# Performance work log

Measured on AMD Instinct MI355X. Metric: run time of the kernel, lower is better.

The kernel has to match this reference:

```python
import jax, jax.numpy as jnp
import numpy as np

N = 100000
E = 3200000
IN_C, NHID, OUT_C, K = 256, 128, 40, 2


def gcn_norm(src, dst, ew, n):
    # add self loops with weight 1.0 (PyG gcn_norm default, add_self_loops=True)
    loop = jnp.arange(n, dtype=src.dtype)
    src = jnp.concatenate([src, loop])
    dst = jnp.concatenate([dst, loop])
    ew = jnp.concatenate([ew, jnp.ones((n,), dtype=ew.dtype)])
    deg = jax.ops.segment_sum(ew, dst, num_segments=n)
    dinv = jnp.where(deg > 0, jax.lax.rsqrt(deg), 0.0)
    norm = dinv[src] * ew * dinv[dst]
    return src, dst, norm


def sgconv(x, src, dst, norm, W, b, k, n):
    # x' = (D^-1/2 (A+I) D^-1/2)^k x, then linear
    for _ in range(k):
        x = jax.ops.segment_sum(x[src] * norm[:, None], dst, num_segments=n)
    return x @ W + b


def setup_inputs() -> dict:
    key = jax.random.key(0)
    ks = jax.random.split(key, 8)
    x = jax.random.normal(ks[0], (N, IN_C), dtype=jnp.float32)
    edge_index = jax.random.randint(ks[1], (2, E), 0, N, dtype=jnp.int64)
    edge_weight = jax.random.uniform(ks[2], (E,), dtype=jnp.float32)
    s1 = 1.0 / np.sqrt(IN_C)
    s2 = 1.0 / np.sqrt(NHID)
    W1 = jax.random.uniform(ks[3], (IN_C, NHID), minval=-s1, maxval=s1, dtype=jnp.float32)
    b1 = jax.random.uniform(ks[4], (NHID,), minval=-s1, maxval=s1, dtype=jnp.float32)
    W2 = jax.random.uniform(ks[5], (NHID, OUT_C), minval=-s2, maxval=s2, dtype=jnp.float32)
    b2 = jax.random.uniform(ks[6], (OUT_C,), minval=-s2, maxval=s2, dtype=jnp.float32)
    return {"x": x, "edge_index": edge_index, "edge_weight": edge_weight,
            "W1": W1, "b1": b1, "W2": W2, "b2": b2}


def reference(x, edge_index, edge_weight, W1, b1, W2, b2):
    n = x.shape[0]
    src, dst, norm = gcn_norm(edge_index[0], edge_index[1], edge_weight, n)
    h = jax.nn.relu(sgconv(x, src, dst, norm, W1, b1, K, n))
    # dropout is identity in eval mode (training=False)
    out = sgconv(h, src, dst, norm, W2, b2, K, n)
    return jax.nn.log_softmax(out, axis=1)
```

## Files before the change

kernel.cpp:

```cpp
#include <hip/hip_runtime.h>
#include <math.h>


constexpr int IN_C = 256, NHID = 128, OUT_C = 40;
constexpr int BSHIFT = 8;
constexpr int BNODES = 256;
constexpr int BCAP = 16128;
constexpr int MAXB = 400;
typedef unsigned int u32;
typedef unsigned short u16;
typedef unsigned char u8;
typedef __attribute__((ext_vector_type(8))) short bf16x8;
typedef __attribute__((ext_vector_type(4))) float f32x4;

__device__ inline u16 f2bf(float f) {
    u32 u = __float_as_uint(f);
    return (u16)((u + 0x7FFF + ((u >> 16) & 1)) >> 16);
}
__device__ inline int nlo4(u32 v) { return ((int)(v << 28)) >> 28; }
__device__ inline int nhi4(u32 v) { return ((int)(v << 24)) >> 28; }

__global__ __launch_bounds__(256) void k_bucketize(const int* __restrict__ src,
                                                   const int* __restrict__ dst,
                                                   const float* __restrict__ ew,
                                                   int* __restrict__ bcur,
                                                   int2* __restrict__ bbuf,
                                                   int E, int nbins) {
    __shared__ int hist[MAXB];
    __shared__ int base[MAXB];
    int tid = threadIdx.x;
    int chunk = (E + gridDim.x - 1) / gridDim.x;
    int e0 = blockIdx.x * chunk;
    int e1 = min(E, e0 + chunk);
    for (int i = tid; i < nbins; i += 256) hist[i] = 0;
    __syncthreads();
    for (int e = e0 + tid; e < e1; e += 256)
        atomicAdd(&hist[dst[e] >> BSHIFT], 1);
    __syncthreads();
    for (int i = tid; i < nbins; i += 256) {
        int c = hist[i];
        base[i] = c ? atomicAdd(&bcur[i], c) : 0;
        hist[i] = 0;
    }
    __syncthreads();
    for (int e = e0 + tid; e < e1; e += 256) {
        int d = dst[e];
        int b = d >> BSHIFT;
        int r = atomicAdd(&hist[b], 1);
        int pos = base[b] + r;
        if (pos < BCAP) {
            int meta = src[e] | ((d & (BNODES - 1)) << 17);
            bbuf[(size_t)b * BCAP + pos] = make_int2(meta, __float_as_int(ew[e]));
        }
    }
}

__global__ __launch_bounds__(256) void k_bcnt_deg(const int2* __restrict__ bbuf,
                                                  const int* __restrict__ bcur,
                                                  int* __restrict__ cnt,
                                                  float* __restrict__ dinv,
                                                  float* __restrict__ selfnorm, int N) {
    __shared__ int hist[BNODES];
    __shared__ int dsum[BNODES];
    int b = blockIdx.x;
    int tid = threadIdx.x;
    hist[tid] = 0; dsum[tid] = 0;
    __syncthreads();
    int c = min(bcur[b], BCAP);
    const int2* p = bbuf + (size_t)b * BCAP;
    for (int e = tid; e < c; e += 256) {
        int2 rec = p[e];
        int dl = rec.x >> 17;
        atomicAdd(&hist[dl], 1);
        atomicAdd(&dsum[dl], (int)rintf(__int_as_float(rec.y) * 8388608.0f));
    }
    __syncthreads();
    int node = b * BNODES + tid;
    if (node < N) {
        cnt[node] = hist[tid];
        float d = (float)dsum[tid] * (1.0f / 8388608.0f) + 1.0f;
        dinv[node] = rsqrtf(d);
        selfnorm[node] = 1.0f / d;
    }
}

__global__ __launch_bounds__(256) void k_scan_part(const int* __restrict__ cnt,
                                                   int* __restrict__ partial, int N) {
    __shared__ int sh[256];
    int i = blockIdx.x * 256 + threadIdx.x;
    sh[threadIdx.x] = (i < N) ? cnt[i] : 0;
    __syncthreads();
    for (int off = 128; off > 0; off >>= 1) {
        if (threadIdx.x < off) sh[threadIdx.x] += sh[threadIdx.x + off];
        __syncthreads();
    }
    if (threadIdx.x == 0) partial[blockIdx.x] = sh[0];
}

__global__ __launch_bounds__(512) void k_scan_top(int* __restrict__ partial, int nb) {
    __shared__ int sh[512];
    int t = threadIdx.x;
    int v = (t < nb) ? partial[t] : 0;
    sh[t] = v;
    __syncthreads();
    for (int off = 1; off < 512; off <<= 1) {
        int add = (t >= off) ? sh[t - off] : 0;
        __syncthreads();
        sh[t] += add;
        __syncthreads();
    }
    if (t < nb) partial[t] = sh[t] - v;
}

__global__ __launch_bounds__(256) void k_scan_apply(const int* __restrict__ cnt,
                                                    const int* __restrict__ partial,
                                                    int* __restrict__ row_start, int N) {
    __shared__ int sh[256];
    int i = blockIdx.x * 256 + threadIdx.x;
    int v = (i < N) ? cnt[i] : 0;
    sh[threadIdx.x] = v;
    __syncthreads();
    for (int off = 1; off < 256; off <<= 1) {
        int add = (threadIdx.x >= off) ? sh[threadIdx.x - off] : 0;
        __syncthreads();
        sh[threadIdx.x] += add;
        __syncthreads();
    }
    if (i < N) row_start[i] = sh[threadIdx.x] - v + partial[blockIdx.x];
}

__global__ __launch_bounds__(256) void k_place(const int2* __restrict__ bbuf,
                                               const int* __restrict__ bcur,
                                               const int* __restrict__ row_start,
                                               const float* __restrict__ dinv,
                                               int2* __restrict__ csr, int N) {
    __shared__ int rs[BNODES];
    __shared__ int cur[BNODES];
    __shared__ float dv[BNODES];
    int b = blockIdx.x;
    int tid = threadIdx.x;
    int node = b * BNODES + tid;
    rs[tid] = (node < N) ? row_start[node] : 0;
    dv[tid] = (node < N) ? dinv[node] : 0.f;
    cur[tid] = 0;
    __syncthreads();
    int c = min(bcur[b], BCAP);
    const int2* p = bbuf + (size_t)b * BCAP;
    for (int e = tid; e < c; e += 256) {
        int2 rec = p[e];
        int dl = rec.x >> 17;
        int s = rec.x & 0x1FFFF;
        float w = dinv[s] * __int_as_float(rec.y) * dv[dl];
        int r = atomicAdd(&cur[dl], 1);
        csr[rs[dl] + r] = make_int2(s, __float_as_int(w));
    }
}

__global__ __launch_bounds__(256) void k_wconv(const float* __restrict__ W,
                                               u16* __restrict__ Wc) {
    int o = blockIdx.x * 256 + threadIdx.x;
    if (o < IN_C * NHID) {
        int j = o & 7, col = (o >> 3) & 127, c = o >> 10;
        Wc[o] = f2bf(W[(size_t)(c * 8 + j) * NHID + col]);
    }
}

__global__ __launch_bounds__(256) void k_gmax(const float* __restrict__ v, int n,
                                              int* __restrict__ gm) {
    __shared__ float sm[4];
    float m = 0.f;
    for (int i = blockIdx.x * 256 + threadIdx.x; i < n; i += 256 * 256)
        m = fmaxf(m, v[i]);
#pragma unroll
    for (int o = 32; o > 0; o >>= 1) m = fmaxf(m, __shfl_xor(m, o, 64));
    if ((threadIdx.x & 63) == 0) sm[threadIdx.x >> 6] = m;
    __syncthreads();
    if (threadIdx.x == 0) {
        m = fmaxf(fmaxf(sm[0], sm[1]), fmaxf(sm[2], sm[3]));
        atomicMax(gm, __float_as_int(m));
    }
}

__global__ __launch_bounds__(256) void k_gemm1(const float* __restrict__ X,
                                               const u16* __restrict__ Wc,
                                               u16* __restrict__ Yq,
                                               float* __restrict__ Ys, int N) {
    int tid = threadIdx.x;
    int wv = tid >> 6, lane = tid & 63;
    int q = lane >> 4, r16 = lane & 15;
    int row = blockIdx.x * 64 + wv * 16 + r16;
    int rowc = min(row, N - 1);
    const float* xp = X + (size_t)rowc * IN_C + q * 8;
    f32x4 acc[8];
#pragma unroll
    for (int i = 0; i < 8; ++i) acc[i] = (f32x4){0.f, 0.f, 0.f, 0.f};
#pragma unroll
    for (int ks = 0; ks < 8; ++ks) {
        float4 a0 = *(const float4*)(xp + ks * 32);
        float4 a1 = *(const float4*)(xp + ks * 32 + 4);
        bf16x8 xf;
        xf[0] = (short)f2bf(a0.x); xf[1] = (short)f2bf(a0.y);
        xf[2] = (short)f2bf(a0.z); xf[3] = (short)f2bf(a0.w);
        xf[4] = (short)f2bf(a1.x); xf[5] = (short)f2bf(a1.y);
        xf[6] = (short)f2bf(a1.z); xf[7] = (short)f2bf(a1.w);
        int c = ks * 4 + q;
#pragma unroll
        for (int ct = 0; ct < 8; ++ct) {
            bf16x8 wf = *(const bf16x8*)&Wc[(size_t)((c << 7) + ct * 16 + r16) << 3];
            acc[ct] = __builtin_amdgcn_mfma_f32_16x16x32_bf16(wf, xf, acc[ct], 0, 0, 0);
        }
    }
    float m = 0.f;
#pragma unroll
    for (int ct = 0; ct < 8; ++ct) {
        m = fmaxf(m, fmaxf(fmaxf(fabsf(acc[ct].x), fabsf(acc[ct].y)),
                           fmaxf(fabsf(acc[ct].z), fabsf(acc[ct].w))));
    }
    m = fmaxf(m, __shfl_xor(m, 16, 64));
    m = fmaxf(m, __shfl_xor(m, 32, 64));
    float qs = m > 0.f ? 7.0f / m : 0.f;
    if (row < N) {
        u16* yp = Yq + (size_t)row * 32;
#pragma unroll
        for (int ct = 0; ct < 8; ++ct) {
            int q0 = (int)rintf(acc[ct].x * qs);
            int q1 = (int)rintf(acc[ct].y * qs);
            int q2 = (int)rintf(acc[ct].z * qs);
            int q3 = (int)rintf(acc[ct].w * qs);
            u32 b0 = (q0 & 0xF) | ((q1 & 0xF) << 4);
            u32 b1_ = (q2 & 0xF) | ((q3 & 0xF) << 4);
            yp[ct * 4 + q] = (u16)(b0 | (b1_ << 8));
        }
        if (lane < 16) Ys[row] = m * (1.0f / 7.0f);
    }
}

__global__ __launch_bounds__(256) void k_gemm2(const u32* __restrict__ Hq,
                                               const float* __restrict__ Hs,
                                               const float* __restrict__ W2,
                                               const float* __restrict__ b1,
                                               u8* __restrict__ Tq,
                                               float* __restrict__ Ts, int N) {
    __shared__ float Ws[NHID * OUT_C];
    __shared__ float As[64][132];
    __shared__ float b1s[128];
    int tid = threadIdx.x;
    for (int idx = tid; idx < NHID * OUT_C; idx += 256) Ws[idx] = W2[idx];
    if (tid < 128) b1s[tid] = b1[tid];
    __syncthreads();
    int bm = blockIdx.x * 64;
#pragma unroll
    for (int j = 0; j < 4; ++j) {
        int idx = tid + j * 256;
        int r = idx >> 4, w = idx & 15;
        int grow = bm + r;
        float vals[8] = {};
        if (grow < N) {
            u32 v = Hq[(size_t)grow * 16 + w];
            float s = Hs[grow];
#pragma unroll
            for (int k = 0; k < 4; ++k) {
                u32 byte = (v >> (8 * k)) & 0xFF;
                vals[2 * k]     = s * (float)nlo4(byte);
                vals[2 * k + 1] = s * (float)nhi4(byte);
            }
        }
#pragma unroll
        for (int k = 0; k < 8; ++k)
            As[r][w * 8 + k] = fmaxf(vals[k] + b1s[w * 8 + k], 0.f);
    }
    __syncthreads();
    int r = tid >> 2;
    int c0 = (tid & 3) * 10;
    float acc[10] = {};
#pragma unroll 4
    for (int k = 0; k < NHID; ++k) {
        float a = As[r][k];
#pragma unroll
        for (int j = 0; j < 10; ++j) acc[j] += a * Ws[k * OUT_C + c0 + j];
    }
    float m = 0.f;
#pragma unroll
    for (int j = 0; j < 10; ++j) m = fmaxf(m, fabsf(acc[j]));
    m = fmaxf(m, __shfl_xor(m, 1, 64));
    m = fmaxf(m, __shfl_xor(m, 2, 64));
    float qs = m > 0.f ? 7.0f / m : 0.f;
    int grow = bm + r;
    if (grow < N) {
        u8* tp = Tq + (size_t)grow * 32 + (tid & 3) * 5;
#pragma unroll
        for (int j = 0; j < 5; ++j) {
            int q0 = (int)rintf(acc[2 * j] * qs);
            int q1 = (int)rintf(acc[2 * j + 1] * qs);
            tp[j] = (u8)((q0 & 0xF) | ((q1 & 0xF) << 4));
        }
        if ((tid & 3) == 0) Ts[grow] = m * (1.0f / 7.0f);
    }
}

__global__ __launch_bounds__(256) void k_prop128(const u8* __restrict__ in,
                                                 const float* __restrict__ ins,
                                                 u8* __restrict__ outq,
                                                 float* __restrict__ outs,
                                                 const int2* __restrict__ csr,
                                                 const int* __restrict__ row_start,
                                                 const int* __restrict__ cnt,
                                                 const float* __restrict__ selfnorm,
                                                 const int* __restrict__ gmaxi, int N) {
    __shared__ int2 stage[256];
    int tid = threadIdx.x;
    int wid = (blockIdx.x * 256 + tid) >> 6;
    int lane = tid & 63;
    int wb = tid & ~63;
    if (wid >= N) return;
    float gm = __int_as_float(*gmaxi);
    float S = gm > 0.f ? 524288.0f / gm : 0.f;
    float invS = gm * (1.0f / 524288.0f);
    int beg = row_start[wid], num = cnt[wid];
    int wqs = (int)rintf(selfnorm[wid] * ins[wid] * S);
    u32 xv = in[(size_t)wid * 64 + lane];
    int ax = wqs * nlo4(xv), ay = wqs * nhi4(xv);
    int bx = 0, by = 0;
    int e = beg, end = beg + num;
    while (e < end) {
        int m = min(64, end - e);
        int2 rec = csr[e + min(lane, m - 1)];
        int wq = (int)rintf(__int_as_float(rec.y) * ins[rec.x] * S);
        stage[wb + lane] = make_int2(rec.x, wq);
        int j = 0;
        for (; j + 8 <= m; j += 8) {
            int2 r0 = stage[wb + j + 0];
            int2 r1 = stage[wb + j + 1];
            int2 r2 = stage[wb + j + 2];
            int2 r3 = stage[wb + j + 3];
            int2 r4 = stage[wb + j + 4];
            int2 r5 = stage[wb + j + 5];
            int2 r6 = stage[wb + j + 6];
            int2 r7 = stage[wb + j + 7];
            u32 x0 = in[(size_t)r0.x * 64 + lane];
            u32 x1 = in[(size_t)r1.x * 64 + lane];
            u32 x2 = in[(size_t)r2.x * 64 + lane];
            u32 x3 = in[(size_t)r3.x * 64 + lane];
            u32 x4 = in[(size_t)r4.x * 64 + lane];
            u32 x5 = in[(size_t)r5.x * 64 + lane];
            u32 x6 = in[(size_t)r6.x * 64 + lane];
            u32 x7 = in[(size_t)r7.x * 64 + lane];
            ax += r0.y * nlo4(x0); ay += r0.y * nhi4(x0);
            bx += r1.y * nlo4(x1); by += r1.y * nhi4(x1);
            ax += r2.y * nlo4(x2); ay += r2.y * nhi4(x2);
            bx += r3.y * nlo4(x3); by += r3.y * nhi4(x3);
            ax += r4.y * nlo4(x4); ay += r4.y * nhi4(x4);
            bx += r5.y * nlo4(x5); by += r5.y * nhi4(x5);
            ax += r6.y * nlo4(x6); ay += r6.y * nhi4(x6);
            bx += r7.y * nlo4(x7); by += r7.y * nhi4(x7);
        }
        for (; j < m; ++j) {
            int2 r = stage[wb + j];
            u32 x = in[(size_t)r.x * 64 + lane];
            ax += r.y * nlo4(x); ay += r.y * nhi4(x);
        }
        e += m;
    }
    ax += bx; ay += by;
    float axf = (float)ax * invS, ayf = (float)ay * invS;
    float m2 = fmaxf(fabsf(axf), fabsf(ayf));
#pragma unroll
    for (int o = 32; o > 0; o >>= 1) m2 = fmaxf(m2, __shfl_xor(m2, o, 64));
    float qs = m2 > 0.f ? 7.0f / m2 : 0.f;
    int qx = (int)rintf(axf * qs), qy = (int)rintf(ayf * qs);
    outq[(size_t)wid * 64 + lane] = (u8)((qx & 0xF) | ((qy & 0xF) << 4));
    if (lane == 0) outs[wid] = m2 * (1.0f / 7.0f);
}

__device__ inline void prop40_body(const u8* __restrict__ in,
                                   const float* __restrict__ ins,
                                   const int2* __restrict__ csr,
                                   const int* __restrict__ row_start,
                                   const int* __restrict__ cnt,
                                   const float* __restrict__ selfnorm,
                                   int2* stage, int wb,
                                   int wid, int lane, float S,
                                   int& axo, int& ayo) {
    int half = lane >> 5, fl = lane & 31;
    bool act = fl < 20;
    int beg = row_start[wid], end = beg + cnt[wid];
    int ax = 0, ay = 0, bx = 0, by = 0;
    if (act && half == 0) {
        u32 u = in[(size_t)wid * 32 + fl];
        int wqs = (int)rintf(selfnorm[wid] * ins[wid] * S);
        ax = wqs * nlo4(u); ay = wqs * nhi4(u);
    }
    int e = beg;
    while (e < end) {
        int m = min(64, end - e);
        int2 rec = csr[e + min(lane, m - 1)];
        int wq = (int)rintf(__int_as_float(rec.y) * ins[rec.x] * S);
        stage[wb + lane] = make_int2(rec.x, wq);
        int j = 0;
        for (; j + 8 <= m; j += 8) {
            int2 r0 = stage[wb + j + half];
            int2 r1 = stage[wb + j + 2 + half];
            int2 r2 = stage[wb + j + 4 + half];
            int2 r3 = stage[wb + j + 6 + half];
            if (act) {
                u32 u0 = in[(size_t)r0.x * 32 + fl];
                u32 u1 = in[(size_t)r1.x * 32 + fl];
                u32 u2 = in[(size_t)r2.x * 32 + fl];
                u32 u3 = in[(size_t)r3.x * 32 + fl];
                ax += r0.y * nlo4(u0); ay += r0.y * nhi4(u0);
                bx += r1.y * nlo4(u1); by += r1.y * nhi4(u1);
                ax += r2.y * nlo4(u2); ay += r2.y * nhi4(u2);
                bx += r3.y * nlo4(u3); by += r3.y * nhi4(u3);
            }
        }
        for (; j + half < m; j += 2) {
            int2 r = stage[wb + j + half];
            if (act) {
                u32 u = in[(size_t)r.x * 32 + fl];
                ax += r.y * nlo4(u); ay += r.y * nhi4(u);
            }
        }
        e += m;
    }
    ax += bx; ay += by;
    ax += __shfl_xor(ax, 32, 64);
    ay += __shfl_xor(ay, 32, 64);
    axo = ax; ayo = ay;
}

__global__ __launch_bounds__(256) void k_prop40(const u8* __restrict__ in,
                                                const float* __restrict__ ins,
                                                u8* __restrict__ outq,
                                                float* __restrict__ outs,
                                                const int2* __restrict__ csr,
                                                const int* __restrict__ row_start,
                                                const int* __restrict__ cnt,
                                                const float* __restrict__ selfnorm,
                                                const int* __restrict__ gmaxi, int N) {
    __shared__ int2 stage[256];
    int tid = threadIdx.x;
    int wid = (blockIdx.x * 256 + tid) >> 6;
    int lane = tid & 63;
    if (wid >= N) return;
    float gm = __int_as_float(*gmaxi);
    float S = gm > 0.f ? 524288.0f / gm : 0.f;
    float invS = gm * (1.0f / 524288.0f);
    int ax, ay;
    prop40_body(in, ins, csr, row_start, cnt, selfnorm, stage, tid & ~63, wid, lane, S, ax, ay);
    int half = lane >> 5, fl = lane & 31;
    float axf = (float)ax * invS, ayf = (float)ay * invS;
    float m2 = fmaxf(fabsf(axf), fabsf(ayf));
    if (fl >= 20) m2 = 0.f;
#pragma unroll
    for (int o = 16; o > 0; o >>= 1) m2 = fmaxf(m2, __shfl_xor(m2, o, 64));
    float qs = m2 > 0.f ? 7.0f / m2 : 0.f;
    if (half == 0 && fl < 20) {
        int qx = (int)rintf(axf * qs), qy = (int)rintf(ayf * qs);
        outq[(size_t)wid * 32 + fl] = (u8)((qx & 0xF) | ((qy & 0xF) << 4));
        if (fl == 0) outs[wid] = m2 * (1.0f / 7.0f);
    }
}

__global__ __launch_bounds__(256) void k_prop40_lsm(const u8* __restrict__ in,
                                                    const float* __restrict__ ins,
                                                    float* __restrict__ out,
                                                    const int2* __restrict__ csr,
                                                    const int* __restrict__ row_start,
                                                    const int* __restrict__ cnt,
                                                    const float* __restrict__ selfnorm,
                                                    const float* __restrict__ b2,
                                                    const int* __restrict__ gmaxi, int N) {
    __shared__ int2 stage[256];
    int tid = threadIdx.x;
    int wid = (blockIdx.x * 256 + tid) >> 6;
    int lane = tid & 63;
    if (wid >= N) return;
    float gm = __int_as_float(*gmaxi);
    float S = gm > 0.f ? 524288.0f / gm : 0.f;
    float invS = gm * (1.0f / 524288.0f);
    int ax, ay;
    prop40_body(in, ins, csr, row_start, cnt, selfnorm, stage, tid & ~63, wid, lane, S, ax, ay);
    int half = lane >> 5, fl = lane & 31;
    bool act = fl < 20;
    float vx = -INFINITY, vy = -INFINITY;
    if (half == 0 && act) {
        vx = (float)ax * invS + b2[2 * fl];
        vy = (float)ay * invS + b2[2 * fl + 1];
    }
    float m2 = fmaxf(vx, vy);
#pragma unroll
    for (int o = 32; o > 0; o >>= 1) m2 = fmaxf(m2, __shfl_xor(m2, o, 64));
    float ex = (half == 0 && act) ? (__expf(vx - m2) + __expf(vy - m2)) : 0.f;
    float s = ex;
#pragma unroll
    for (int o = 32; o > 0; o >>= 1) s += __shfl_xor(s, o, 64);
    if (half == 0 && act) {
        float ls = logf(s);
        float2 o2 = make_float2(vx - m2 - ls, vy - m2 - ls);
        *(float2*)&out[(size_t)wid * 40 + 2 * fl] = o2;
    }
}

extern "C" void kernel_launch(void* const* d_in, const int* in_sizes, int n_in,
                              void* d_out, int out_size, void* d_ws, size_t ws_size,
                              hipStream_t stream) {
    const int N = in_sizes[0] / IN_C;
    const int E = in_sizes[2];
    const float* x  = (const float*)d_in[0];
    const int*   src = (const int*)d_in[1];
    const int*   dst = src + E;
    const float* ew = (const float*)d_in[2];
    const float* W1 = (const float*)d_in[3];
    const float* b1 = (const float*)d_in[4];
    const float* W2 = (const float*)d_in[5];
    const float* b2 = (const float*)d_in[6];
    float* out = (float*)d_out;

    char* p = (char*)d_ws;
    auto alloc = [&](size_t bytes) -> char* {
        char* r = p;
        p += (bytes + 255) & ~(size_t)255;
        return r;
    };
    float* dinv     = (float*)alloc((size_t)N * 4);
    float* selfnorm = (float*)alloc((size_t)N * 4);
    int*   cnt      = (int*)alloc((size_t)N * 4);
    int*   row_start= (int*)alloc((size_t)N * 4);
    int*   partial  = (int*)alloc(((N + 255) / 256) * 4);
    int*   bcur     = (int*)alloc(MAXB * 4);
    int*   gmax     = (int*)alloc(8 * 4);
    u16*   Wc       = (u16*)alloc((size_t)IN_C * NHID * 2);
    int2*  csr      = (int2*)alloc((size_t)E * 8);
    const int nbins = (N + BNODES - 1) >> BSHIFT;
    char*  region   = alloc((size_t)nbins * BCAP * 8);
    int2*  bbuf = (int2*)region;
    u8*    h4A  = (u8*)(region);
    u8*    h4B  = (u8*)(region + 7000000);
    u8*    t4A  = (u8*)(region + 14000000);
    u8*    t4B  = (u8*)(region + 17400000);
    float* sA   = (float*)(region + 20800000);
    float* sB   = (float*)(region + 21300000);
    float* tsA  = (float*)(region + 21800000);
    float* tsB  = (float*)(region + 22300000);

    hipMemsetAsync(bcur, 0, nbins * 4, stream);
    hipMemsetAsync(gmax, 0, 8 * 4, stream);

    int gn = (N + 255) / 256;
    int nb = gn;
    int gp = (N + 3) / 4;

    k_bucketize<<<256, 256, 0, stream>>>(src, dst, ew, bcur, bbuf, E, nbins);
    k_bcnt_deg<<<nbins, 256, 0, stream>>>(bbuf, bcur, cnt, dinv, selfnorm, N);
    k_scan_part<<<nb, 256, 0, stream>>>(cnt, partial, N);
    k_scan_top<<<1, 512, 0, stream>>>(partial, nb);
    k_scan_apply<<<nb, 256, 0, stream>>>(cnt, partial, row_start, N);
    k_place<<<nbins, 256, 0, stream>>>(bbuf, bcur, row_start, dinv, csr, N);
    k_wconv<<<(IN_C * NHID + 255) / 256, 256, 0, stream>>>(W1, Wc);

    k_gemm1<<<(N + 63) / 64, 256, 0, stream>>>(x, Wc, (u16*)h4A, sA, N);
    k_gmax<<<256, 256, 0, stream>>>(sA, N, &gmax[0]);

    k_prop128<<<gp, 256, 0, stream>>>(h4A, sA, h4B, sB, csr, row_start, cnt, selfnorm,
                                      &gmax[0], N);
    k_gmax<<<256, 256, 0, stream>>>(sB, N, &gmax[1]);
    k_prop128<<<gp, 256, 0, stream>>>(h4B, sB, h4A, sA, csr, row_start, cnt, selfnorm,
                                      &gmax[1], N);

    k_gemm2<<<(N + 63) / 64, 256, 0, stream>>>((const u32*)h4A, sA, W2, b1, t4A, tsA, N);
    k_gmax<<<256, 256, 0, stream>>>(tsA, N, &gmax[2]);

    k_prop40<<<gp, 256, 0, stream>>>(t4A, tsA, t4B, tsB, csr, row_start, cnt, selfnorm,
                                     &gmax[2], N);
    k_gmax<<<256, 256, 0, stream>>>(tsB, N, &gmax[3]);
    k_prop40_lsm<<<gp, 256, 0, stream>>>(t4B, tsB, out, csr, row_start, cnt, selfnorm, b2,
                                         &gmax[3], N);
}
```

Baseline: 500.1 us.

## Stage bucketized edges in LDS and widen prop128 gathers to 4-byte loads

The bucketize kernel now computes a local prefix over bin histograms, sorts its edge chunk into shared memory by bin, and then writes each bin's records to global memory contiguously, replacing scattered global stores with coalesced runs. The 128-wide propagation kernel splits each wavefront into four groups of 16 lanes. Each lane loads 4 bytes (8 int4 features) per neighbor, so four edges are processed per iteration, and partial sums are combined with cross-group shuffles. The aim is fewer, wider gather transactions and better store coalescing. The cost is a large shared-memory footprint (about 125 KB per block) that limits occupancy, plus extra shuffle reductions.

```diff
diff --git a/kernel.cpp b/kernel.cpp
--- a/kernel.cpp
+++ b/kernel.cpp
@@ -7,6 +7,7 @@
 constexpr int BNODES = 256;
 constexpr int BCAP = 16128;
 constexpr int MAXB = 400;
+constexpr int CHUNK = 12544;
 typedef unsigned int u32;
 typedef unsigned short u16;
 typedef unsigned char u8;
@@ -26,32 +27,55 @@
                                                    int* __restrict__ bcur,
                                                    int2* __restrict__ bbuf,
                                                    int E, int nbins) {
+    __shared__ int2 recs[CHUNK];
+    __shared__ u16 rbin[CHUNK];
     __shared__ int hist[MAXB];
-    __shared__ int base[MAXB];
+    __shared__ int lbase[MAXB];
+    __shared__ int gbase[MAXB];
+    __shared__ int cur[MAXB];
     int tid = threadIdx.x;
     int chunk = (E + gridDim.x - 1) / gridDim.x;
     int e0 = blockIdx.x * chunk;
     int e1 = min(E, e0 + chunk);
-    for (int i = tid; i < nbins; i += 256) hist[i] = 0;
+    int n = e1 - e0;
+    for (int i = tid; i < nbins; i += 256) { hist[i] = 0; cur[i] = 0; }
     __syncthreads();
     for (int e = e0 + tid; e < e1; e += 256)
         atomicAdd(&hist[dst[e] >> BSHIFT], 1);
     __syncthreads();
+    if (tid < 64) {
+        int run = 0;
+        for (int c0 = 0; c0 < nbins; c0 += 64) {
+            int i = c0 + tid;
+            int v = (i < nbins) ? hist[i] : 0;
+            int x = v;
+            for (int o = 1; o < 64; o <<= 1) {
+                int y = __shfl_up(x, o, 64);
+                if (tid >= o) x += y;
+            }
+            if (i < nbins) lbase[i] = run + x - v;
+            run += __shfl(x, 63, 64);
+        }
+    }
+    __syncthreads();
     for (int i = tid; i < nbins; i += 256) {
         int c = hist[i];
-        base[i] = c ? atomicAdd(&bcur[i], c) : 0;
-        hist[i] = 0;
+        gbase[i] = c ? atomicAdd(&bcur[i], c) : 0;
     }
     __syncthreads();
     for (int e = e0 + tid; e < e1; e += 256) {
         int d = dst[e];
         int b = d >> BSHIFT;
-        int r = atomicAdd(&hist[b], 1);
-        int pos = base[b] + r;
-        if (pos < BCAP) {
-            int meta = src[e] | ((d & (BNODES - 1)) << 17);
-            bbuf[(size_t)b * BCAP + pos] = make_int2(meta, __float_as_int(ew[e]));
-        }
+        int r = atomicAdd(&cur[b], 1);
+        int loff = lbase[b] + r;
+        recs[loff] = make_int2(src[e] | ((d & (BNODES - 1)) << 17), __float_as_int(ew[e]));
+        rbin[loff] = (u16)b;
+    }
+    __syncthreads();
+    for (int i = tid; i < n; i += 256) {
+        int b = rbin[i];
+        int gpos = gbase[b] + (i - lbase[b]);
+        if (gpos < BCAP) bbuf[(size_t)b * BCAP + gpos] = recs[i];
     }
 }
 
@@ -316,59 +340,48 @@
     float gm = __int_as_float(*gmaxi);
     float S = gm > 0.f ? 524288.0f / gm : 0.f;
     float invS = gm * (1.0f / 524288.0f);
+    int g = lane >> 4;
+    int c4 = (lane & 15) * 4;
     int beg = row_start[wid], num = cnt[wid];
     int wqs = (int)rintf(selfnorm[wid] * ins[wid] * S);
-    u32 xv = in[(size_t)wid * 64 + lane];
-    int ax = wqs * nlo4(xv), ay = wqs * nhi4(xv);
-    int bx = 0, by = 0;
+    int acc[8] = {};
+    {
+        u32 x = *(const u32*)(in + (size_t)wid * 64 + c4);
+        int w = (g == 0) ? wqs : 0;
+#pragma unroll
+        for (int k = 0; k < 8; ++k) acc[k] += w * ((int)(x << (28 - 4 * k)) >> 28);
+    }
     int e = beg, end = beg + num;
     while (e < end) {
         int m = min(64, end - e);
         int2 rec = csr[e + min(lane, m - 1)];
         int wq = (int)rintf(__int_as_float(rec.y) * ins[rec.x] * S);
-        stage[wb + lane] = make_int2(rec.x, wq);
-        int j = 0;
-        for (; j + 8 <= m; j += 8) {
-            int2 r0 = stage[wb + j + 0];
-            int2 r1 = stage[wb + j + 1];
-            int2 r2 = stage[wb + j + 2];
-            int2 r3 = stage[wb + j + 3];
-            int2 r4 = stage[wb + j + 4];
-            int2 r5 = stage[wb + j + 5];
-            int2 r6 = stage[wb + j + 6];
-            int2 r7 = stage[wb + j + 7];
-            u32 x0 = in[(size_t)r0.x * 64 + lane];
-            u32 x1 = in[(size_t)r1.x * 64 + lane];
-            u32 x2 = in[(size_t)r2.x * 64 + lane];
-            u32 x3 = in[(size_t)r3.x * 64 + lane];
-            u32 x4 = in[(size_t)r4.x * 64 + lane];
-            u32 x5 = in[(size_t)r5.x * 64 + lane];
-            u32 x6 = in[(size_t)r6.x * 64 + lane];
-            u32 x7 = in[(size_t)r7.x * 64 + lane];
-            ax += r0.y * nlo4(x0); ay += r0.y * nhi4(x0);
-            bx += r1.y * nlo4(x1); by += r1.y * nhi4(x1);
-            ax += r2.y * nlo4(x2); ay += r2.y * nhi4(x2);
-            bx += r3.y * nlo4(x3); by += r3.y * nhi4(x3);
-            ax += r4.y * nlo4(x4); ay += r4.y * nhi4(x4);
-            bx += r5.y * nlo4(x5); by += r5.y * nhi4(x5);
-            ax += r6.y * nlo4(x6); ay += r6.y * nhi4(x6);
-            bx += r7.y * nlo4(x7); by += r7.y * nhi4(x7);
-        }
-        for (; j < m; ++j) {
-            int2 r = stage[wb + j];
-            u32 x = in[(size_t)r.x * 64 + lane];
-            ax += r.y * nlo4(x); ay += r.y * nhi4(x);
+        if (lane >= m) wq = 0;
+        stage[wb + lane] = make_int2(rec.x << 6, wq);
+        for (int j = 0; j < m; j += 4) {
+            int2 r = stage[wb + j + g];
+            u32 x = *(const u32*)(in + (size_t)(u32)r.x + c4);
+#pragma unroll
+            for (int k = 0; k < 8; ++k) acc[k] += r.y * ((int)(x << (28 - 4 * k)) >> 28);
         }
         e += m;
     }
-    ax += bx; ay += by;
-    float axf = (float)ax * invS, ayf = (float)ay * invS;
-    float m2 = fmaxf(fabsf(axf), fabsf(ayf));
-#pragma unroll
-    for (int o = 32; o > 0; o >>= 1) m2 = fmaxf(m2, __shfl_xor(m2, o, 64));
+#pragma unroll
+    for (int k = 0; k < 8; ++k) {
+        acc[k] += __shfl_xor(acc[k], 16, 64);
+        acc[k] += __shfl_xor(acc[k], 32, 64);
+    }
+    float f[8]; float mloc = 0.f;
+#pragma unroll
+    for (int k = 0; k < 8; ++k) { f[k] = (float)acc[k] * invS; mloc = fmaxf(mloc, fabsf(f[k])); }
+    float m2 = mloc;
+#pragma unroll
+    for (int o = 8; o > 0; o >>= 1) m2 = fmaxf(m2, __shfl_xor(m2, o, 64));
     float qs = m2 > 0.f ? 7.0f / m2 : 0.f;
-    int qx = (int)rintf(axf * qs), qy = (int)rintf(ayf * qs);
-    outq[(size_t)wid * 64 + lane] = (u8)((qx & 0xF) | ((qy & 0xF) << 4));
+    u32 w = 0;
+#pragma unroll
+    for (int k = 0; k < 8; ++k) { int q = (int)rintf(f[k] * qs); w |= (u32)(q & 0xF) << (4 * k); }
+    if (lane < 16) *(u32*)(outq + (size_t)wid * 64 + c4) = w;
     if (lane == 0) outs[wid] = m2 * (1.0f / 7.0f);
 }
 
```

After: 511.4 us. 1.02x slower.
